# Optimization experiments

Measured on AMD Instinct MI355X. Metric: run time of the kernel, lower is better.

Reference implementation:

```python
import jax, jax.numpy as jnp
import numpy as np

EPS = 1e-5
NHEAD = 8

def layer_norm(x, g, b):
    mu = jnp.mean(x, axis=-1, keepdims=True)
    var = jnp.mean((x - mu) ** 2, axis=-1, keepdims=True)
    return (x - mu) * jax.lax.rsqrt(var + EPS) * g + b

def setup_inputs() -> dict:
    key = jax.random.key(0)
    ks = jax.random.split(key, 8)
    B, S, D, F = 4, 2048, 512, 2048
    s = 0.02
    return {
        "x": jax.random.normal(ks[0], (B, S, D), jnp.float32),
        "Wqkv": jax.random.normal(ks[1], (3 * D, D), jnp.float32) * s,
        "bqkv": jnp.zeros((3 * D,), jnp.float32),
        "Wo": jax.random.normal(ks[2], (D, D), jnp.float32) * s,
        "bo": jnp.zeros((D,), jnp.float32),
        "W1": jax.random.normal(ks[3], (F, D), jnp.float32) * s,
        "b1": jnp.zeros((F,), jnp.float32),
        "W2": jax.random.normal(ks[4], (D, F), jnp.float32) * s,
        "b2": jnp.zeros((D,), jnp.float32),
        "g1": jnp.ones((D,), jnp.float32),
        "bn1": jnp.zeros((D,), jnp.float32),
        "g2": jnp.ones((D,), jnp.float32),
        "bn2": jnp.zeros((D,), jnp.float32),
    }

def reference(x, Wqkv, bqkv, Wo, bo, W1, b1, W2, b2, g1, bn1, g2, bn2):
    B, S, D = x.shape
    H = NHEAD
    hd = D // H
    # fused QKV projection (torch MultiheadAttention in_proj)
    qkv = x @ Wqkv.T + bqkv                      # [B,S,3D]
    q, k, v = jnp.split(qkv, 3, axis=-1)
    q = q.reshape(B, S, H, hd).transpose(0, 2, 1, 3)  # [B,H,S,hd]
    k = k.reshape(B, S, H, hd).transpose(0, 2, 1, 3)
    v = v.reshape(B, S, H, hd).transpose(0, 2, 1, 3)
    scores = jnp.einsum("bhqd,bhkd->bhqk", q, k) / jnp.sqrt(jnp.float32(hd))
    causal = jnp.tril(jnp.ones((S, S), bool))
    scores = jnp.where(causal, scores, jnp.float32(-jnp.inf))
    attn = jax.nn.softmax(scores, axis=-1)
    ctx = jnp.einsum("bhqk,bhkd->bhqd", attn, v)        # [B,H,S,hd]
    ctx = ctx.transpose(0, 2, 1, 3).reshape(B, S, D)
    attn_out = ctx @ Wo.T + bo
    # residual + LayerNorm 1
    x = layer_norm(x + attn_out, g1, bn1)
    # FFN (ReLU) + residual + LayerNorm 2
    ff = jax.nn.relu(x @ W1.T + b1) @ W2.T + b2
    x = layer_norm(x + ff, g2, bn2)
    return x
```

## Files before the change

kernel.cpp:

```cpp
#include <hip/hip_runtime.h>
#include <hip/hip_bf16.h>
#include <math.h>

#define D_MODEL 512
#define SEQ     2048
#define BATCH   4
#define NHEADS  8
#define HDIM    64
#define FFN     2048
#define TOKENS  (BATCH*SEQ)

typedef __attribute__((ext_vector_type(8))) short bf16x8;
typedef __attribute__((ext_vector_type(4))) float f32x4;
typedef __attribute__((ext_vector_type(4))) unsigned u32x4;

__device__ inline ushort f2bf(float f) {
    unsigned u = __builtin_bit_cast(unsigned, f);
    unsigned r = (u + 0x7fffu + ((u >> 16) & 1u)) >> 16;
    return (ushort)r;
}

#define GLOAD_LDS16(g, l) __builtin_amdgcn_global_load_lds( \
    (const __attribute__((address_space(1))) void*)(g), \
    (__attribute__((address_space(3))) void*)(l), 16, 0, 0)

__global__ void cast_all_bf16(const float* __restrict__ x, const float* __restrict__ Wqkv,
                              const float* __restrict__ Wo, const float* __restrict__ W1,
                              const float* __restrict__ W2, ushort* __restrict__ outbase) {
    const int i = blockIdx.x * blockDim.x + threadIdx.x;
    if (i >= 1835008) return;
    float4 v;
    if      (i < 1048576) v = ((const float4*)x)[i];
    else if (i < 1245184) v = ((const float4*)Wqkv)[i - 1048576];
    else if (i < 1310720) v = ((const float4*)Wo)[i - 1245184];
    else if (i < 1572864) v = ((const float4*)W1)[i - 1310720];
    else                  v = ((const float4*)W2)[i - 1572864];
    ushort4 o;
    o.x = f2bf(v.x); o.y = f2bf(v.y); o.z = f2bf(v.z); o.w = f2bf(v.w);
    ((ushort4*)outbase)[i] = o;
}

template<int MODE, int RELU, int BM, int BN>
__global__ __launch_bounds__(BN == 256 ? 512 : 256)
void gemm_bt_mfma(const ushort* __restrict__ A,
                  const ushort* __restrict__ W,
                  const float* __restrict__ bias,
                  void* __restrict__ CoutA,
                  ushort* __restrict__ Qc,
                  ushort* __restrict__ Kc,
                  ushort* __restrict__ Vt,
                  int M, int N, int Kstride, int Klen) {
    constexpr int NW    = (BN == 256) ? 8 : 4;
    constexpr int WC    = NW / 2;
    constexpr int MI    = BM / 32;
    constexpr int AROWS = BM / NW;
    constexpr bool A2   = (AROWS == 32);
    __shared__ ushort Asb[3][BM * 32];
    __shared__ ushort Bsb[3][BN * 32];

    const int tid  = threadIdx.x;
    const int lane = tid & 63;
    const int wv   = tid >> 6;

    const int Gx = gridDim.x;
    const int f  = blockIdx.x + Gx * blockIdx.y;
    const int xc = f & 7;
    const int j  = f >> 3;
    const int ni = j % Gx;
    const int mi = xc * (gridDim.y >> 3) + j / Gx;
    const int m0 = mi * BM;
    const int n0 = ni * BN;

    const int wm = (wv / WC) * (BM / 2);
    const int wn = (wv % WC) * 64;

    const int rA = wv * AROWS + (lane >> 2);
    const int rB = wv * 32 + (lane >> 2);
    const int cS = (((lane & 3) ^ ((lane >> 3) & 3)) * 8);
    const ushort* gA0 = A + (size_t)(m0 + rA) * Kstride + cS;
    const ushort* gA1 = gA0 + (size_t)16 * Kstride;
    const ushort* gB0 = W + (size_t)(n0 + rB) * Kstride + cS;
    const ushort* gB1 = gB0 + (size_t)16 * Kstride;

    f32x4 acc[MI][4] = {};

    const int fr  = lane & 15;
    const int fks = (((lane >> 4) ^ ((fr >> 1) & 3)) * 8);
    const int loA = wv * (AROWS * 32);
    const int loB = wv * 1024;

#define STAGE(ab, bb) do { \
        GLOAD_LDS16(gA0, (ab) + loA); \
        if constexpr (A2) GLOAD_LDS16(gA1, (ab) + loA + 512); \
        GLOAD_LDS16(gB0, (bb) + loB); \
        GLOAD_LDS16(gB1, (bb) + loB + 512); \
        gA0 += 32; if constexpr (A2) gA1 += 32; \
        gB0 += 32; gB1 += 32; } while (0)

#define COMPUTE(ab, bb) do { \
        bf16x8 af_[MI], bf_[4]; \
        _Pragma("unroll") \
        for (int i_ = 0; i_ < MI; ++i_) \
            af_[i_] = *(const bf16x8*)((ab) + (wm + i_ * 16 + fr) * 32 + fks); \
        _Pragma("unroll") \
        for (int j_ = 0; j_ < 4; ++j_) \
            bf_[j_] = *(const bf16x8*)((bb) + (wn + j_ * 16 + fr) * 32 + fks); \
        _Pragma("unroll") \
        for (int i_ = 0; i_ < MI; ++i_) \
            _Pragma("unroll") \
            for (int j_ = 0; j_ < 4; ++j_) \
                acc[i_][j_] = __builtin_amdgcn_mfma_f32_16x16x32_bf16(af_[i_], bf_[j_], acc[i_][j_], 0, 0, 0); \
        } while (0)

#define PWAIT do { \
        if constexpr (A2) asm volatile("s_waitcnt vmcnt(4)" ::: "memory"); \
        else              asm volatile("s_waitcnt vmcnt(3)" ::: "memory"); \
        __builtin_amdgcn_s_barrier(); \
        __builtin_amdgcn_sched_barrier(0); } while (0)

    ushort *Ac = Asb[0], *An = Asb[1], *As = Asb[2];
    ushort *Bc = Bsb[0], *Bn = Bsb[1], *Bs = Bsb[2];

    STAGE(Ac, Bc);
    STAGE(An, Bn);
    const int ntiles = Klen >> 5;
    for (int t = 0; t < ntiles - 1; ++t) {
        PWAIT;
        if (t + 2 < ntiles) STAGE(As, Bs);
        COMPUTE(Ac, Bc);
        ushort* tA = Ac; Ac = An; An = As; As = tA;
        ushort* tB = Bc; Bc = Bn; Bn = Bs; Bs = tB;
    }
    asm volatile("s_waitcnt vmcnt(0)" ::: "memory");
    __builtin_amdgcn_s_barrier();
    __builtin_amdgcn_sched_barrier(0);
    COMPUTE(Ac, Bc);

#undef STAGE
#undef COMPUTE
#undef PWAIT

    const int col  = lane & 15;
    const int rowq = (lane >> 4) * 4;
    #pragma unroll
    for (int i = 0; i < MI; ++i) {
        const int gm = m0 + wm + i * 16 + rowq;
        #pragma unroll
        for (int j2 = 0; j2 < 4; ++j2) {
            const int gn = n0 + wn + j2 * 16 + col;
            if (MODE == 2) {
                const float bv = bias[gn];
                const int seg = gn >> 9;
                const int h   = (gn >> 6) & 7;
                const int dd  = gn & 63;
                const int bb  = gm >> 11;
                const int ss  = gm & 2047;
                const int bh  = bb * 8 + h;
                if (seg == 2) {
                    ushort4 pk;
                    pk.x = f2bf(acc[i][j2][0] + bv);
                    pk.y = f2bf(acc[i][j2][1] + bv);
                    pk.z = f2bf(acc[i][j2][2] + bv);
                    pk.w = f2bf(acc[i][j2][3] + bv);
                    *(ushort4*)(Vt + ((size_t)bh * 64 + dd) * 2048 + ss) = pk;
                } else {
                    ushort* dst = (seg == 0 ? Qc : Kc) + ((size_t)bh * 2048 + ss) * 64 + dd;
                    #pragma unroll
                    for (int r = 0; r < 4; ++r)
                        dst[(size_t)r * 64] = f2bf(acc[i][j2][r] + bv);
                }
            } else if (MODE == 3) {
                float* dst = (float*)CoutA;
                const float bv = bias[gn];
                #pragma unroll
                for (int r = 0; r < 4; ++r)
                    dst[(size_t)(gm + r) * N + gn] = acc[i][j2][r] + bv;
            } else {
                const float bv = bias[gn];
                #pragma unroll
                for (int r = 0; r < 4; ++r) {
                    float v = acc[i][j2][r] + bv;
                    if (RELU) v = fmaxf(v, 0.f);
                    ((ushort*)CoutA)[(size_t)(gm + r) * N + gn] = f2bf(v);
                }
            }
        }
    }
}

__device__ __forceinline__ void attn_step(const ushort* __restrict__ Kb,
                                          const ushort* __restrict__ Vb,
                                          bf16x8 qf0, bf16x8 qf1,
                                          float& lp, f32x4 (&o)[4],
                                          int qw, int j0, bool diag,
                                          int col, int g, int c7) {
    f32x4 s[4] = {};
    __builtin_amdgcn_s_setprio(1);
    #pragma unroll
    for (int nt = 0; nt < 4; ++nt) {
        const int kr = nt * 16 + col;
        bf16x8 kf0 = *(const bf16x8*)(Kb + kr * 64 + (((g    ) ^ c7) * 8));
        bf16x8 kf1 = *(const bf16x8*)(Kb + kr * 64 + (((g + 4) ^ c7) * 8));
        s[nt] = __builtin_amdgcn_mfma_f32_16x16x32_bf16(kf0, qf0, s[nt], 0, 0, 0);
        s[nt] = __builtin_amdgcn_mfma_f32_16x16x32_bf16(kf1, qf1, s[nt], 0, 0, 0);
    }
    __builtin_amdgcn_s_setprio(0);

    if (diag) {
        #pragma unroll
        for (int nt = 0; nt < 4; ++nt)
            #pragma unroll
            for (int r = 0; r < 4; ++r)
                if ((j0 + nt * 16 + 4 * g + r) > (qw + col)) s[nt][r] = -INFINITY;
    }

    unsigned W[8];
    #pragma unroll
    for (int nt = 0; nt < 4; ++nt) {
        float p0 = __expf(s[nt][0] * 0.125f);
        float p1 = __expf(s[nt][1] * 0.125f);
        float p2 = __expf(s[nt][2] * 0.125f);
        float p3 = __expf(s[nt][3] * 0.125f);
        lp += (p0 + p1) + (p2 + p3);
        asm("v_cvt_pk_bf16_f32 %0, %1, %2" : "=v"(W[2 * nt])     : "v"(p0), "v"(p1));
        asm("v_cvt_pk_bf16_f32 %0, %1, %2" : "=v"(W[2 * nt + 1]) : "v"(p2), "v"(p3));
    }
    asm("v_permlane32_swap_b32 %0, %1" : "+v"(W[0]), "+v"(W[2]));
    asm("v_permlane32_swap_b32 %0, %1" : "+v"(W[1]), "+v"(W[3]));
    asm("v_permlane32_swap_b32 %0, %1" : "+v"(W[4]), "+v"(W[6]));
    asm("v_permlane32_swap_b32 %0, %1" : "+v"(W[5]), "+v"(W[7]));
    asm("v_permlane16_swap_b32 %0, %1" : "+v"(W[0]), "+v"(W[2]));
    asm("v_permlane16_swap_b32 %0, %1" : "+v"(W[1]), "+v"(W[3]));
    asm("v_permlane16_swap_b32 %0, %1" : "+v"(W[4]), "+v"(W[6]));
    asm("v_permlane16_swap_b32 %0, %1" : "+v"(W[5]), "+v"(W[7]));

    u32x4 wa = {W[0], W[1], W[2], W[3]};
    u32x4 wb = {W[4], W[5], W[6], W[7]};
    bf16x8 pf0 = __builtin_bit_cast(bf16x8, wa);
    bf16x8 pf1 = __builtin_bit_cast(bf16x8, wb);

    __builtin_amdgcn_s_setprio(1);
    #pragma unroll
    for (int nt = 0; nt < 4; ++nt) {
        const int vr = nt * 16 + col;
        bf16x8 vf0 = *(const bf16x8*)(Vb + vr * 64 + (((g    ) ^ c7) * 8));
        bf16x8 vf1 = *(const bf16x8*)(Vb + vr * 64 + (((g + 4) ^ c7) * 8));
        o[nt] = __builtin_amdgcn_mfma_f32_16x16x32_bf16(pf0, vf0, o[nt], 0, 0, 0);
        o[nt] = __builtin_amdgcn_mfma_f32_16x16x32_bf16(pf1, vf1, o[nt], 0, 0, 0);
    }
    __builtin_amdgcn_s_setprio(0);
}

__global__ __launch_bounds__(256, 4) void attn_mfma_kernel(const ushort* __restrict__ Qc,
                                                           const ushort* __restrict__ Kc,
                                                           const ushort* __restrict__ Vt,
                                                           ushort* __restrict__ ctxb) {
    __shared__ ushort Ks[2 * 64 * 64];
    __shared__ ushort Vs[2 * 64 * 64];

    const int tid  = threadIdx.x;
    const int lane = tid & 63;
    const int wv   = tid >> 6;
    const int idx  = blockIdx.x;
    const int bh   = (idx & 7) * 4 + (idx >> 7);
    const int pair = (idx >> 3) & 15;
    const int q0a  = pair * 64;
    const int q0b  = (31 - pair) * 64;
    const int qwA  = q0a + wv * 16;
    const int qwB  = q0b + wv * 16;

    const int col = lane & 15;
    const int g   = lane >> 4;
    const int c7  = col & 7;

    bf16x8 qfA0, qfA1, qfB0, qfB1;
    {
        const ushort* qa = Qc + ((size_t)bh * 2048 + qwA + col) * 64 + g * 8;
        qfA0 = *(const bf16x8*)qa;
        qfA1 = *(const bf16x8*)(qa + 32);
        const ushort* qb = Qc + ((size_t)bh * 2048 + qwB + col) * 64 + g * 8;
        qfB0 = *(const bf16x8*)qb;
        qfB1 = *(const bf16x8*)(qb + 32);
    }

    const int srow = tid >> 2;
    const int sch  = 2 * (tid & 3);
    const ushort* Kg = Kc + ((size_t)bh * 2048 + srow) * 64 + sch * 8;
    const ushort* Vg = Vt + ((size_t)bh * 64 + srow) * 2048 + sch * 8;
    const int ko0 = srow * 64 + (((sch    ) ^ (srow & 7)) * 8);
    const int ko1 = srow * 64 + (((sch + 1) ^ (srow & 7)) * 8);

    float lpa = 0.f, lpb = 0.f;
    f32x4 oa[4] = {}, ob[4] = {};

    bf16x8 pk0 = *(const bf16x8*)(Kg);
    bf16x8 pk1 = *(const bf16x8*)(Kg + 8);
    bf16x8 pv0 = *(const bf16x8*)(Vg);
    bf16x8 pv1 = *(const bf16x8*)(Vg + 8);

    for (int j0 = 0; j0 <= q0b; j0 += 64) {
        const int par = (j0 >> 6) & 1;
        ushort* Kb = Ks + par * 4096;
        ushort* Vb = Vs + par * 4096;
        *(bf16x8*)(Kb + ko0) = pk0; *(bf16x8*)(Kb + ko1) = pk1;
        *(bf16x8*)(Vb + ko0) = pv0; *(bf16x8*)(Vb + ko1) = pv1;
        __syncthreads();

        if (j0 < q0b) {
            pk0 = *(const bf16x8*)(Kg + (size_t)(j0 + 64) * 64);
            pk1 = *(const bf16x8*)(Kg + (size_t)(j0 + 64) * 64 + 8);
            pv0 = *(const bf16x8*)(Vg + j0 + 64);
            pv1 = *(const bf16x8*)(Vg + j0 + 72);
        }

        if (j0 <= q0a)
            attn_step(Kb, Vb, qfA0, qfA1, lpa, oa, qwA, j0, j0 == q0a, col, g, c7);
        attn_step(Kb, Vb, qfB0, qfB1, lpb, ob, qwB, j0, j0 == q0b, col, g, c7);
    }

    float la = lpa; la += __shfl_xor(la, 16); la += __shfl_xor(la, 32);
    float lb = lpb; lb += __shfl_xor(lb, 16); lb += __shfl_xor(lb, 32);
    const int b = bh >> 3, h = bh & 7;
    #pragma unroll
    for (int r = 0; r < 4; ++r) {
        const float inva = 1.f / __shfl(la, 4 * g + r);
        const float invb = 1.f / __shfl(lb, 4 * g + r);
        const size_t rowa = ((size_t)b * 2048 + qwA + 4 * g + r) * 512 + h * 64;
        const size_t rowb = ((size_t)b * 2048 + qwB + 4 * g + r) * 512 + h * 64;
        #pragma unroll
        for (int nt = 0; nt < 4; ++nt) {
            ctxb[rowa + nt * 16 + col] = f2bf(oa[nt][r] * inva);
            ctxb[rowb + nt * 16 + col] = f2bf(ob[nt][r] * invb);
        }
    }
}

template<int WRITE_BF16>
__global__ void ln_residual(const float* __restrict__ A, const float* __restrict__ B1,
                            const float* __restrict__ g, const float* __restrict__ beta,
                            float* __restrict__ out, ushort* __restrict__ outb) {
    __shared__ float sbuf[8];
    const int row = blockIdx.x;
    const int tid = threadIdx.x;
    const size_t base = (size_t)row * D_MODEL;

    float v0 = A[base + tid]       + B1[base + tid];
    float v1 = A[base + tid + 256] + B1[base + tid + 256];

    float sum = v0 + v1;
    #pragma unroll
    for (int off = 32; off; off >>= 1) sum += __shfl_xor(sum, off);
    if ((tid & 63) == 0) sbuf[tid >> 6] = sum;
    __syncthreads();
    if (tid == 0) { float t = 0.f; for (int i = 0; i < 4; ++i) t += sbuf[i]; sbuf[4] = t; }
    __syncthreads();
    const float mu = sbuf[4] * (1.f / 512.f);
    __syncthreads();

    float d0 = v0 - mu, d1 = v1 - mu;
    float sq = d0 * d0 + d1 * d1;
    #pragma unroll
    for (int off = 32; off; off >>= 1) sq += __shfl_xor(sq, off);
    if ((tid & 63) == 0) sbuf[tid >> 6] = sq;
    __syncthreads();
    if (tid == 0) { float t = 0.f; for (int i = 0; i < 4; ++i) t += sbuf[i]; sbuf[4] = t; }
    __syncthreads();
    const float var = sbuf[4] * (1.f / 512.f);
    const float rs  = rsqrtf(var + 1e-5f);

    float r0 = d0 * rs * g[tid]       + beta[tid];
    float r1 = d1 * rs * g[tid + 256] + beta[tid + 256];
    out[base + tid]       = r0;
    out[base + tid + 256] = r1;
    if (WRITE_BF16) {
        outb[base + tid]       = f2bf(r0);
        outb[base + tid + 256] = f2bf(r1);
    }
}

extern "C" void kernel_launch(void* const* d_in, const int* in_sizes, int n_in,
                              void* d_out, int out_size, void* d_ws, size_t ws_size,
                              hipStream_t stream) {
    const float* x    = (const float*)d_in[0];
    const float* Wqkv = (const float*)d_in[1];
    const float* bqkv = (const float*)d_in[2];
    const float* Wo   = (const float*)d_in[3];
    const float* bo   = (const float*)d_in[4];
    const float* W1   = (const float*)d_in[5];
    const float* b1   = (const float*)d_in[6];
    const float* W2   = (const float*)d_in[7];
    const float* b2   = (const float*)d_in[8];
    const float* g1   = (const float*)d_in[9];
    const float* bn1  = (const float*)d_in[10];
    const float* g2   = (const float*)d_in[11];
    const float* bn2  = (const float*)d_in[12];

    float* ws = (float*)d_ws;
    ushort* Qcb     = (ushort*)ws;
    ushort* Kcb     = (ushort*)(ws + 2097152);
    ushort* Vtb     = (ushort*)(ws + 4194304);
    ushort* ff1b    = (ushort*)ws;
    float*  ff2a    = ws + 8388608;
    float*  attn_a  = ws + 12582912;
    float*  ln1     = ws + 16777216;
    ushort* ctxb  = (ushort*)(ws + 20971520);
    ushort* ln1b  = (ushort*)(ws + 23068672);
    ushort* xb    = (ushort*)(ws + 25165824);
    ushort* Wqkvb = (ushort*)(ws + 27262976);
    float*  out   = (float*)d_out;
    ushort* W1b   = (ushort*)(ws + 27787264);
    ushort* W2b   = (ushort*)(ws + 28311552);
    ushort* Wob   = (ushort*)(ws + 27656192);

    const dim3 blk(256);

    cast_all_bf16<<<dim3(7168), blk, 0, stream>>>(x, Wqkv, Wo, W1, W2, xb);

    gemm_bt_mfma<2,0,128,128><<<dim3(1536/128, 8192/128), blk, 0, stream>>>(
        xb, Wqkvb, bqkv, nullptr, Qcb, Kcb, Vtb, TOKENS, 1536, 512, 512);
    attn_mfma_kernel<<<dim3(512), blk, 0, stream>>>(Qcb, Kcb, Vtb, ctxb);
    gemm_bt_mfma<3,0,64,128><<<dim3(512/128, 8192/64), blk, 0, stream>>>(
        ctxb, Wob, bo, attn_a, nullptr, nullptr, nullptr, TOKENS, 512, 512, 512);
    ln_residual<1><<<dim3(TOKENS), blk, 0, stream>>>(x, attn_a, g1, bn1, ln1, ln1b);
    gemm_bt_mfma<1,1,128,256><<<dim3(2048/256, 8192/128), dim3(512), 0, stream>>>(
        ln1b, W1b, b1, ff1b, nullptr, nullptr, nullptr, TOKENS, 2048, 512, 512);
    gemm_bt_mfma<3,0,64,128><<<dim3(512/128, 8192/64), blk, 0, stream>>>(
        ff1b, W2b, b2, ff2a, nullptr, nullptr, nullptr, TOKENS, 512, 2048, 2048);
    ln_residual<0><<<dim3(TOKENS), blk, 0, stream>>>(ln1, ff2a, g2, bn2, out, nullptr);
}
```

Before: 239.4 us.

## Use direct global-to-LDS async loads in attention, share K/V fragments, warp-per-row LayerNorm

The attention kernel now stages K/V tiles with global_load_lds directly into double-buffered shared memory, replacing register staging, and uses a single barrier per tile. Each step loads K and V fragments once and reuses them for both query blocks, with launch bounds relaxed to 2 blocks per CU to fit the extra registers. LayerNorm is rewritten so one wavefront handles each row with float4 loads and shuffle-only reductions, dropping the shared-memory barriers and launching a quarter as many blocks. The risks are lower occupancy in attention and a reliance on vmcnt waits being correct for the LDS-direct loads.

```diff
diff --git a/kernel.cpp b/kernel.cpp
--- a/kernel.cpp
+++ b/kernel.cpp
@@ -188,70 +188,131 @@
     }
 }
 
-__device__ __forceinline__ void attn_step(const ushort* __restrict__ Kb,
-                                          const ushort* __restrict__ Vb,
-                                          bf16x8 qf0, bf16x8 qf1,
-                                          float& lp, f32x4 (&o)[4],
-                                          int qw, int j0, bool diag,
-                                          int col, int g, int c7) {
-    f32x4 s[4] = {};
-    __builtin_amdgcn_s_setprio(1);
+__device__ __forceinline__ void attn_step2(const ushort* __restrict__ Kb,
+                                           const ushort* __restrict__ Vb,
+                                           bf16x8 qfA0, bf16x8 qfA1,
+                                           bf16x8 qfB0, bf16x8 qfB1,
+                                           float& lpa, float& lpb,
+                                           f32x4 (&oa)[4], f32x4 (&ob)[4],
+                                           int qwA, int qwB, int j0,
+                                           int q0a, int q0b,
+                                           int col, int g, int c7) {
+    const bool doA = (j0 <= q0a);
+
+    bf16x8 kf0[4], kf1[4];
     #pragma unroll
     for (int nt = 0; nt < 4; ++nt) {
         const int kr = nt * 16 + col;
-        bf16x8 kf0 = *(const bf16x8*)(Kb + kr * 64 + (((g    ) ^ c7) * 8));
-        bf16x8 kf1 = *(const bf16x8*)(Kb + kr * 64 + (((g + 4) ^ c7) * 8));
-        s[nt] = __builtin_amdgcn_mfma_f32_16x16x32_bf16(kf0, qf0, s[nt], 0, 0, 0);
-        s[nt] = __builtin_amdgcn_mfma_f32_16x16x32_bf16(kf1, qf1, s[nt], 0, 0, 0);
+        kf0[nt] = *(const bf16x8*)(Kb + kr * 64 + (((g    ) ^ c7) * 8));
+        kf1[nt] = *(const bf16x8*)(Kb + kr * 64 + (((g + 4) ^ c7) * 8));
+    }
+
+    f32x4 sA[4] = {}, sB[4] = {};
+    __builtin_amdgcn_s_setprio(1);
+    #pragma unroll
+    for (int nt = 0; nt < 4; ++nt) {
+        sB[nt] = __builtin_amdgcn_mfma_f32_16x16x32_bf16(kf0[nt], qfB0, sB[nt], 0, 0, 0);
+        sB[nt] = __builtin_amdgcn_mfma_f32_16x16x32_bf16(kf1[nt], qfB1, sB[nt], 0, 0, 0);
+    }
+    if (doA) {
+        #pragma unroll
+        for (int nt = 0; nt < 4; ++nt) {
+            sA[nt] = __builtin_amdgcn_mfma_f32_16x16x32_bf16(kf0[nt], qfA0, sA[nt], 0, 0, 0);
+            sA[nt] = __builtin_amdgcn_mfma_f32_16x16x32_bf16(kf1[nt], qfA1, sA[nt], 0, 0, 0);
+        }
     }
     __builtin_amdgcn_s_setprio(0);
 
-    if (diag) {
+    bf16x8 vf0[4], vf1[4];
+    #pragma unroll
+    for (int nt = 0; nt < 4; ++nt) {
+        const int vr = nt * 16 + col;
+        vf0[nt] = *(const bf16x8*)(Vb + vr * 64 + (((g    ) ^ c7) * 8));
+        vf1[nt] = *(const bf16x8*)(Vb + vr * 64 + (((g + 4) ^ c7) * 8));
+    }
+
+    if (j0 == q0b) {
         #pragma unroll
         for (int nt = 0; nt < 4; ++nt)
             #pragma unroll
             for (int r = 0; r < 4; ++r)
-                if ((j0 + nt * 16 + 4 * g + r) > (qw + col)) s[nt][r] = -INFINITY;
-    }
-
-    unsigned W[8];
+                if ((j0 + nt * 16 + 4 * g + r) > (qwB + col)) sB[nt][r] = -INFINITY;
+    }
+    unsigned WB[8];
     #pragma unroll
     for (int nt = 0; nt < 4; ++nt) {
-        float p0 = __expf(s[nt][0] * 0.125f);
-        float p1 = __expf(s[nt][1] * 0.125f);
-        float p2 = __expf(s[nt][2] * 0.125f);
-        float p3 = __expf(s[nt][3] * 0.125f);
-        lp += (p0 + p1) + (p2 + p3);
-        asm("v_cvt_pk_bf16_f32 %0, %1, %2" : "=v"(W[2 * nt])     : "v"(p0), "v"(p1));
-        asm("v_cvt_pk_bf16_f32 %0, %1, %2" : "=v"(W[2 * nt + 1]) : "v"(p2), "v"(p3));
-    }
-    asm("v_permlane32_swap_b32 %0, %1" : "+v"(W[0]), "+v"(W[2]));
-    asm("v_permlane32_swap_b32 %0, %1" : "+v"(W[1]), "+v"(W[3]));
-    asm("v_permlane32_swap_b32 %0, %1" : "+v"(W[4]), "+v"(W[6]));
-    asm("v_permlane32_swap_b32 %0, %1" : "+v"(W[5]), "+v"(W[7]));
-    asm("v_permlane16_swap_b32 %0, %1" : "+v"(W[0]), "+v"(W[2]));
-    asm("v_permlane16_swap_b32 %0, %1" : "+v"(W[1]), "+v"(W[3]));
-    asm("v_permlane16_swap_b32 %0, %1" : "+v"(W[4]), "+v"(W[6]));
-    asm("v_permlane16_swap_b32 %0, %1" : "+v"(W[5]), "+v"(W[7]));
-
-    u32x4 wa = {W[0], W[1], W[2], W[3]};
-    u32x4 wb = {W[4], W[5], W[6], W[7]};
-    bf16x8 pf0 = __builtin_bit_cast(bf16x8, wa);
-    bf16x8 pf1 = __builtin_bit_cast(bf16x8, wb);
-
-    __builtin_amdgcn_s_setprio(1);
-    #pragma unroll
-    for (int nt = 0; nt < 4; ++nt) {
-        const int vr = nt * 16 + col;
-        bf16x8 vf0 = *(const bf16x8*)(Vb + vr * 64 + (((g    ) ^ c7) * 8));
-        bf16x8 vf1 = *(const bf16x8*)(Vb + vr * 64 + (((g + 4) ^ c7) * 8));
-        o[nt] = __builtin_amdgcn_mfma_f32_16x16x32_bf16(pf0, vf0, o[nt], 0, 0, 0);
-        o[nt] = __builtin_amdgcn_mfma_f32_16x16x32_bf16(pf1, vf1, o[nt], 0, 0, 0);
-    }
-    __builtin_amdgcn_s_setprio(0);
-}
-
-__global__ __launch_bounds__(256, 4) void attn_mfma_kernel(const ushort* __restrict__ Qc,
+        float p0 = __expf(sB[nt][0] * 0.125f);
+        float p1 = __expf(sB[nt][1] * 0.125f);
+        float p2 = __expf(sB[nt][2] * 0.125f);
+        float p3 = __expf(sB[nt][3] * 0.125f);
+        lpb += (p0 + p1) + (p2 + p3);
+        asm("v_cvt_pk_bf16_f32 %0, %1, %2" : "=v"(WB[2 * nt])     : "v"(p0), "v"(p1));
+        asm("v_cvt_pk_bf16_f32 %0, %1, %2" : "=v"(WB[2 * nt + 1]) : "v"(p2), "v"(p3));
+    }
+    asm("v_permlane32_swap_b32 %0, %1" : "+v"(WB[0]), "+v"(WB[2]));
+    asm("v_permlane32_swap_b32 %0, %1" : "+v"(WB[1]), "+v"(WB[3]));
+    asm("v_permlane32_swap_b32 %0, %1" : "+v"(WB[4]), "+v"(WB[6]));
+    asm("v_permlane32_swap_b32 %0, %1" : "+v"(WB[5]), "+v"(WB[7]));
+    asm("v_permlane16_swap_b32 %0, %1" : "+v"(WB[0]), "+v"(WB[2]));
+    asm("v_permlane16_swap_b32 %0, %1" : "+v"(WB[1]), "+v"(WB[3]));
+    asm("v_permlane16_swap_b32 %0, %1" : "+v"(WB[4]), "+v"(WB[6]));
+    asm("v_permlane16_swap_b32 %0, %1" : "+v"(WB[5]), "+v"(WB[7]));
+    {
+        u32x4 wa = {WB[0], WB[1], WB[2], WB[3]};
+        u32x4 wb = {WB[4], WB[5], WB[6], WB[7]};
+        bf16x8 pf0 = __builtin_bit_cast(bf16x8, wa);
+        bf16x8 pf1 = __builtin_bit_cast(bf16x8, wb);
+        __builtin_amdgcn_s_setprio(1);
+        #pragma unroll
+        for (int nt = 0; nt < 4; ++nt) {
+            ob[nt] = __builtin_amdgcn_mfma_f32_16x16x32_bf16(pf0, vf0[nt], ob[nt], 0, 0, 0);
+            ob[nt] = __builtin_amdgcn_mfma_f32_16x16x32_bf16(pf1, vf1[nt], ob[nt], 0, 0, 0);
+        }
+        __builtin_amdgcn_s_setprio(0);
+    }
+
+    if (doA) {
+        if (j0 == q0a) {
+            #pragma unroll
+            for (int nt = 0; nt < 4; ++nt)
+                #pragma unroll
+                for (int r = 0; r < 4; ++r)
+                    if ((j0 + nt * 16 + 4 * g + r) > (qwA + col)) sA[nt][r] = -INFINITY;
+        }
+        unsigned WA[8];
+        #pragma unroll
+        for (int nt = 0; nt < 4; ++nt) {
+            float p0 = __expf(sA[nt][0] * 0.125f);
+            float p1 = __expf(sA[nt][1] * 0.125f);
+            float p2 = __expf(sA[nt][2] * 0.125f);
+            float p3 = __expf(sA[nt][3] * 0.125f);
+            lpa += (p0 + p1) + (p2 + p3);
+            asm("v_cvt_pk_bf16_f32 %0, %1, %2" : "=v"(WA[2 * nt])     : "v"(p0), "v"(p1));
+            asm("v_cvt_pk_bf16_f32 %0, %1, %2" : "=v"(WA[2 * nt + 1]) : "v"(p2), "v"(p3));
+        }
+        asm("v_permlane32_swap_b32 %0, %1" : "+v"(WA[0]), "+v"(WA[2]));
+        asm("v_permlane32_swap_b32 %0, %1" : "+v"(WA[1]), "+v"(WA[3]));
+        asm("v_permlane32_swap_b32 %0, %1" : "+v"(WA[4]), "+v"(WA[6]));
+        asm("v_permlane32_swap_b32 %0, %1" : "+v"(WA[5]), "+v"(WA[7]));
+        asm("v_permlane16_swap_b32 %0, %1" : "+v"(WA[0]), "+v"(WA[2]));
+        asm("v_permlane16_swap_b32 %0, %1" : "+v"(WA[1]), "+v"(WA[3]));
+        asm("v_permlane16_swap_b32 %0, %1" : "+v"(WA[4]), "+v"(WA[6]));
+        asm("v_permlane16_swap_b32 %0, %1" : "+v"(WA[5]), "+v"(WA[7]));
+        u32x4 wa = {WA[0], WA[1], WA[2], WA[3]};
+        u32x4 wb = {WA[4], WA[5], WA[6], WA[7]};
+        bf16x8 pf0 = __builtin_bit_cast(bf16x8, wa);
+        bf16x8 pf1 = __builtin_bit_cast(bf16x8, wb);
+        __builtin_amdgcn_s_setprio(1);
+        #pragma unroll
+        for (int nt = 0; nt < 4; ++nt) {
+            oa[nt] = __builtin_amdgcn_mfma_f32_16x16x32_bf16(pf0, vf0[nt], oa[nt], 0, 0, 0);
+            oa[nt] = __builtin_amdgcn_mfma_f32_16x16x32_bf16(pf1, vf1[nt], oa[nt], 0, 0, 0);
+        }
+        __builtin_amdgcn_s_setprio(0);
+    }
+}
+
+__global__ __launch_bounds__(256, 2) void attn_mfma_kernel(const ushort* __restrict__ Qc,
                                                            const ushort* __restrict__ Kc,
                                                            const ushort* __restrict__ Vt,
                                                            ushort* __restrict__ ctxb) {
@@ -283,40 +344,34 @@
         qfB1 = *(const bf16x8*)(qb + 32);
     }
 
-    const int srow = tid >> 2;
-    const int sch  = 2 * (tid & 3);
-    const ushort* Kg = Kc + ((size_t)bh * 2048 + srow) * 64 + sch * 8;
-    const ushort* Vg = Vt + ((size_t)bh * 64 + srow) * 2048 + sch * 8;
-    const int ko0 = srow * 64 + (((sch    ) ^ (srow & 7)) * 8);
-    const int ko1 = srow * 64 + (((sch + 1) ^ (srow & 7)) * 8);
+    const int l3  = lane >> 3;
+    const int swz = ((lane & 7) ^ l3) * 8;
+    const ushort* KgL = Kc + ((size_t)bh * 2048 + wv * 8 + l3) * 64 + swz;
+    const ushort* VgL = Vt + ((size_t)bh * 64 + wv * 8 + l3) * 2048 + swz;
+    const int dW = wv * 512;
+
+#define ASTAGE(par, jj) do { \
+        GLOAD_LDS16(KgL + (size_t)(jj) * 64,        Ks + (par) * 4096 + dW); \
+        GLOAD_LDS16(KgL + (size_t)(jj) * 64 + 2048, Ks + (par) * 4096 + dW + 2048); \
+        GLOAD_LDS16(VgL + (jj),                     Vs + (par) * 4096 + dW); \
+        GLOAD_LDS16(VgL + (jj) + 65536,             Vs + (par) * 4096 + dW + 2048); } while (0)
 
     float lpa = 0.f, lpb = 0.f;
     f32x4 oa[4] = {}, ob[4] = {};
 
-    bf16x8 pk0 = *(const bf16x8*)(Kg);
-    bf16x8 pk1 = *(const bf16x8*)(Kg + 8);
-    bf16x8 pv0 = *(const bf16x8*)(Vg);
-    bf16x8 pv1 = *(const bf16x8*)(Vg + 8);
-
+    ASTAGE(0, 0);
     for (int j0 = 0; j0 <= q0b; j0 += 64) {
         const int par = (j0 >> 6) & 1;
-        ushort* Kb = Ks + par * 4096;
-        ushort* Vb = Vs + par * 4096;
-        *(bf16x8*)(Kb + ko0) = pk0; *(bf16x8*)(Kb + ko1) = pk1;
-        *(bf16x8*)(Vb + ko0) = pv0; *(bf16x8*)(Vb + ko1) = pv1;
-        __syncthreads();
-
-        if (j0 < q0b) {
-            pk0 = *(const bf16x8*)(Kg + (size_t)(j0 + 64) * 64);
-            pk1 = *(const bf16x8*)(Kg + (size_t)(j0 + 64) * 64 + 8);
-            pv0 = *(const bf16x8*)(Vg + j0 + 64);
-            pv1 = *(const bf16x8*)(Vg + j0 + 72);
-        }
-
-        if (j0 <= q0a)
-            attn_step(Kb, Vb, qfA0, qfA1, lpa, oa, qwA, j0, j0 == q0a, col, g, c7);
-        attn_step(Kb, Vb, qfB0, qfB1, lpb, ob, qwB, j0, j0 == q0b, col, g, c7);
-    }
+        asm volatile("s_waitcnt vmcnt(0)" ::: "memory");
+        __builtin_amdgcn_s_barrier();
+        __builtin_amdgcn_sched_barrier(0);
+        if (j0 < q0b) ASTAGE(par ^ 1, j0 + 64);
+
+        attn_step2(Ks + par * 4096, Vs + par * 4096,
+                   qfA0, qfA1, qfB0, qfB1, lpa, lpb, oa, ob,
+                   qwA, qwB, j0, q0a, q0b, col, g, c7);
+    }
+#undef ASTAGE
 
     float la = lpa; la += __shfl_xor(la, 16); la += __shfl_xor(la, 32);
     float lb = lpb; lb += __shfl_xor(lb, 16); lb += __shfl_xor(lb, 32);
@@ -336,45 +391,50 @@
 }
 
 template<int WRITE_BF16>
-__global__ void ln_residual(const float* __restrict__ A, const float* __restrict__ B1,
+__global__ __launch_bounds__(256) void ln_residual(const float* __restrict__ A,
+                            const float* __restrict__ B1,
                             const float* __restrict__ g, const float* __restrict__ beta,
                             float* __restrict__ out, ushort* __restrict__ outb) {
-    __shared__ float sbuf[8];
-    const int row = blockIdx.x;
-    const int tid = threadIdx.x;
+    const int lane = threadIdx.x & 63;
+    const int row  = blockIdx.x * 4 + (threadIdx.x >> 6);
     const size_t base = (size_t)row * D_MODEL;
-
-    float v0 = A[base + tid]       + B1[base + tid];
-    float v1 = A[base + tid + 256] + B1[base + tid + 256];
-
-    float sum = v0 + v1;
+    const int c0 = lane * 4, c1 = 256 + lane * 4;
+
+    float4 a0 = *(const float4*)&A[base + c0];
+    float4 a1 = *(const float4*)&A[base + c1];
+    float4 b0 = *(const float4*)&B1[base + c0];
+    float4 b1 = *(const float4*)&B1[base + c1];
+    float v0 = a0.x + b0.x, v1 = a0.y + b0.y, v2 = a0.z + b0.z, v3 = a0.w + b0.w;
+    float v4 = a1.x + b1.x, v5 = a1.y + b1.y, v6 = a1.z + b1.z, v7 = a1.w + b1.w;
+
+    float sum = ((v0 + v1) + (v2 + v3)) + ((v4 + v5) + (v6 + v7));
     #pragma unroll
     for (int off = 32; off; off >>= 1) sum += __shfl_xor(sum, off);
-    if ((tid & 63) == 0) sbuf[tid >> 6] = sum;
-    __syncthreads();
-    if (tid == 0) { float t = 0.f; for (int i = 0; i < 4; ++i) t += sbuf[i]; sbuf[4] = t; }
-    __syncthreads();
-    const float mu = sbuf[4] * (1.f / 512.f);
-    __syncthreads();
-
-    float d0 = v0 - mu, d1 = v1 - mu;
-    float sq = d0 * d0 + d1 * d1;
+    const float mu = sum * (1.f / 512.f);
+
+    float d0 = v0 - mu, d1 = v1 - mu, d2 = v2 - mu, d3 = v3 - mu;
+    float d4 = v4 - mu, d5 = v5 - mu, d6 = v6 - mu, d7 = v7 - mu;
+    float sq = ((d0 * d0 + d1 * d1) + (d2 * d2 + d3 * d3))
+             + ((d4 * d4 + d5 * d5) + (d6 * d6 + d7 * d7));
     #pragma unroll
     for (int off = 32; off; off >>= 1) sq += __shfl_xor(sq, off);
-    if ((tid & 63) == 0) sbuf[tid >> 6] = sq;
-    __syncthreads();
-    if (tid == 0) { float t = 0.f; for (int i = 0; i < 4; ++i) t += sbuf[i]; sbuf[4] = t; }
-    __syncthreads();
-    const float var = sbuf[4] * (1.f / 512.f);
-    const float rs  = rsqrtf(var + 1e-5f);
-
-    float r0 = d0 * rs * g[tid]       + beta[tid];
-    float r1 = d1 * rs * g[tid + 256] + beta[tid + 256];
-    out[base + tid]       = r0;
-    out[base + tid + 256] = r1;
+    const float rs = rsqrtf(sq * (1.f / 512.f) + 1e-5f);
+
+    float4 g0 = *(const float4*)&g[c0],    g1 = *(const float4*)&g[c1];
+    float4 e0 = *(const float4*)&beta[c0], e1 = *(const float4*)&beta[c1];
+    float4 r0, r1;
+    r0.x = d0 * rs * g0.x + e0.x; r0.y = d1 * rs * g0.y + e0.y;
+    r0.z = d2 * rs * g0.z + e0.z; r0.w = d3 * rs * g0.w + e0.w;
+    r1.x = d4 * rs * g1.x + e1.x; r1.y = d5 * rs * g1.y + e1.y;
+    r1.z = d6 * rs * g1.z + e1.z; r1.w = d7 * rs * g1.w + e1.w;
+    *(float4*)&out[base + c0] = r0;
+    *(float4*)&out[base + c1] = r1;
     if (WRITE_BF16) {
-        outb[base + tid]       = f2bf(r0);
-        outb[base + tid + 256] = f2bf(r1);
+        ushort4 u0, u1;
+        u0.x = f2bf(r0.x); u0.y = f2bf(r0.y); u0.z = f2bf(r0.z); u0.w = f2bf(r0.w);
+        u1.x = f2bf(r1.x); u1.y = f2bf(r1.y); u1.z = f2bf(r1.z); u1.w = f2bf(r1.w);
+        *(ushort4*)&outb[base + c0] = u0;
+        *(ushort4*)&outb[base + c1] = u1;
     }
 }
 
@@ -421,10 +481,10 @@
     attn_mfma_kernel<<<dim3(512), blk, 0, stream>>>(Qcb, Kcb, Vtb, ctxb);
     gemm_bt_mfma<3,0,64,128><<<dim3(512/128, 8192/64), blk, 0, stream>>>(
         ctxb, Wob, bo, attn_a, nullptr, nullptr, nullptr, TOKENS, 512, 512, 512);
-    ln_residual<1><<<dim3(TOKENS), blk, 0, stream>>>(x, attn_a, g1, bn1, ln1, ln1b);
+    ln_residual<1><<<dim3(TOKENS/4), blk, 0, stream>>>(x, attn_a, g1, bn1, ln1, ln1b);
     gemm_bt_mfma<1,1,128,256><<<dim3(2048/256, 8192/128), dim3(512), 0, stream>>>(
         ln1b, W1b, b1, ff1b, nullptr, nullptr, nullptr, TOKENS, 2048, 512, 512);
     gemm_bt_mfma<3,0,64,128><<<dim3(512/128, 8192/64), blk, 0, stream>>>(
         ff1b, W2b, b2, ff2a, nullptr, nullptr, nullptr, TOKENS, 512, 2048, 2048);
-    ln_residual<0><<<dim3(TOKENS), blk, 0, stream>>>(ln1, ff2a, g2, bn2, out, nullptr);
-}
+    ln_residual<0><<<dim3(TOKENS/4), blk, 0, stream>>>(ln1, ff2a, g2, bn2, out, nullptr);
+}
```

After: 242.2 us. Within noise of the previous version (+1.2%).
